# Optimization experiments

Measured on AMD Instinct MI355X. Metric: run time of the kernel, lower is better.

The kernel has to match this reference:

```python
import jax, jax.numpy as jnp
import numpy as np

N_NODES = 16384
D_IN = 256
D_OUT = 256
AVG_DEG = 32


def setup_inputs() -> dict:
    key = jax.random.key(0)
    kx, ka, kw, kb = jax.random.split(key, 4)
    x = jax.random.normal(kx, (N_NODES, D_IN), dtype=jnp.float32)
    # Binary dense adjacency with average degree ~AVG_DEG (matches `adj[i] > 0` usage).
    adj = (jax.random.uniform(ka, (N_NODES, N_NODES)) < (AVG_DEG / N_NODES)).astype(jnp.float32)
    # nn.Linear(2*in_features, out_features): weight [out, 2*in], bias [out]
    W = jax.random.normal(kw, (D_OUT, 2 * D_IN), dtype=jnp.float32) * (1.0 / np.sqrt(2 * D_IN))
    b = jnp.zeros((D_OUT,), dtype=jnp.float32)
    return {"x": x, "adj": adj, "W": W, "b": b, "sample_size": 10}


def reference(x, adj, W, b, sample_size):
    # Vectorized equivalent of the per-node loop:
    # sample min(deg, sample_size) neighbors uniformly without replacement,
    # mean-aggregate, concat with self features, linear + relu.
    key = jax.random.key(42)
    noise = jax.random.uniform(key, adj.shape)            # [N, N]
    # Gumbel-top-k trick: top-k uniform scores over neighbors == uniform sample w/o replacement.
    scores = jnp.where(adj > 0, noise, -jnp.inf)
    top_scores, top_idx = jax.lax.top_k(scores, sample_size)  # [N, k]
    valid = jnp.isfinite(top_scores)                          # [N, k] false where deg < k
    feats = x[top_idx] * valid[..., None].astype(x.dtype)     # [N, k, d]
    cnt = valid.sum(axis=-1, keepdims=True).astype(x.dtype)   # [N, 1]
    agg = feats.sum(axis=1) / jnp.maximum(cnt, 1.0)           # mean; zeros if no neighbors
    h = jnp.concatenate([x, agg], axis=-1)                    # [N, 2d]
    return jax.nn.relu(h @ W.T + b)
```

## Files before the change

kernel.cpp:

```cpp
#include <hip/hip_runtime.h>
#include <hip/hip_bf16.h>
#include <stdint.h>

#define N_NODES 16384
#define D_IN    256
#define D_OUT   256
#define K_SAMP  10
#define HALF_FLAT (1u << 27)

#define JAX_PARTITIONABLE 1

typedef __attribute__((ext_vector_type(4))) float  f32x4;
typedef __attribute__((ext_vector_type(8))) short  bf16x8;
typedef __attribute__((ext_vector_type(4))) int    i32x4;

__device__ __forceinline__ uint32_t rotl32(uint32_t x, int r) {
    return (x << r) | (x >> (32 - r));
}

__device__ __forceinline__ uint32_t jax_noise_bits(uint32_t r, uint32_t c) {
    const uint32_t i  = (r << 14) | c;
    const uint32_t k0 = 0u, k1 = 42u;
    const uint32_t k2 = 42u ^ 0x1BD11BDAu;
    uint32_t x0, x1;
#if JAX_PARTITIONABLE
    x0 = 0u;
    x1 = i;
#else
    const bool lo = (i < HALF_FLAT);
    x0 = lo ? i : (i - HALF_FLAT);
    x1 = lo ? (i + HALF_FLAT) : i;
#endif
    x0 += k0; x1 += k1;
#define TFR4(a,b,cc,d) \
    x0 += x1; x1 = rotl32(x1,a);  x1 ^= x0; \
    x0 += x1; x1 = rotl32(x1,b);  x1 ^= x0; \
    x0 += x1; x1 = rotl32(x1,cc); x1 ^= x0; \
    x0 += x1; x1 = rotl32(x1,d);  x1 ^= x0;
    TFR4(13,15,26,6);   x0 += k1; x1 += k2 + 1u;
    TFR4(17,29,16,24);  x0 += k2; x1 += k0 + 2u;
    TFR4(13,15,26,6);   x0 += k0; x1 += k1 + 3u;
    TFR4(17,29,16,24);  x0 += k1; x1 += k2 + 4u;
    TFR4(13,15,26,6);   x0 += k2; x1 += k0 + 5u;
#undef TFR4
#if JAX_PARTITIONABLE
    return x0 ^ x1;
#else
    return (i < HALF_FLAT) ? x0 : x1;
#endif
}

__device__ __forceinline__ unsigned short f2bfbits(float f) {
    __hip_bfloat16 h = __float2bfloat16(f);
    return *(unsigned short*)&h;
}

__global__ __launch_bounds__(256) void k_agg(
    const float* __restrict__ x, const float* __restrict__ adj,
    const float* __restrict__ W, unsigned short* __restrict__ Wb,
    unsigned short* __restrict__ h)
{
    const int t    = threadIdx.x;
    const int lane = t & 63;
    const int w    = t >> 6;
    const int r    = blockIdx.x * 4 + w;

    if (blockIdx.x < 128) {
        int i = (blockIdx.x * 256 + t) * 4;
        f32x4 v = *(const f32x4*)(W + i);
        ushort4 u;
        u.x = f2bfbits(v[0]); u.y = f2bfbits(v[1]);
        u.z = f2bfbits(v[2]); u.w = f2bfbits(v[3]);
        *(ushort4*)(Wb + i) = u;
    }

    __shared__ unsigned short candc[4][128];

    const i32x4* rowp = (const i32x4*)(adj + (size_t)r * N_NODES);
    int nc = 0;
    #pragma unroll 8
    for (int it = 0; it < 64; ++it) {
        i32x4 v = __builtin_nontemporal_load(rowp + it * 64 + lane);
        uint32_t any = (uint32_t)v[0] | (uint32_t)v[1] | (uint32_t)v[2] | (uint32_t)v[3];
        unsigned long long m4 = __ballot(any != 0u);
        if (m4) {
            int cb = (it * 64 + lane) * 4;
            #pragma unroll
            for (int j = 0; j < 4; ++j) {
                unsigned long long mask = __ballot(v[j] != 0);
                if (mask) {
                    if (v[j] != 0) {
                        int below = __builtin_amdgcn_mbcnt_hi(
                            (uint32_t)(mask >> 32),
                            __builtin_amdgcn_mbcnt_lo((uint32_t)mask, 0));
                        int slot = nc + below;
                        if (slot < 128) candc[w][slot] = (unsigned short)(cb + j);
                    }
                    nc += __popcll(mask);
                }
            }
        }
    }
    __syncthreads();
    if (nc > 128) nc = 128;

    unsigned long long k0 = 0ull, k1 = 0ull;
    if (lane < nc) {
        uint32_t c   = candc[w][lane];
        uint32_t u23 = jax_noise_bits((uint32_t)r, c) >> 9;
        k0 = ((((unsigned long long)u23) << 14) | (unsigned long long)(16383u - c)) + 1ull;
    }
    if (64 + lane < nc) {
        uint32_t c   = candc[w][64 + lane];
        uint32_t u23 = jax_noise_bits((uint32_t)r, c) >> 9;
        k1 = ((((unsigned long long)u23) << 14) | (unsigned long long)(16383u - c)) + 1ull;
    }

    const int m = nc < K_SAMP ? nc : K_SAMP;
    f32x4 acc = {0.f, 0.f, 0.f, 0.f};
    for (int s = 0; s < m; ++s) {
        unsigned long long my = k0 > k1 ? k0 : k1;
        #pragma unroll
        for (int o = 1; o < 64; o <<= 1) {
            unsigned long long other = __shfl_xor(my, o);
            if (other > my) my = other;
        }
        if (k0 == my) k0 = 0ull; else if (k1 == my) k1 = 0ull;
        const int col = 16383 - (int)((my - 1ull) & 0x3FFFull);
        f32x4 xv = *(const f32x4*)(x + (size_t)col * D_IN + lane * 4);
        acc += xv;
    }
    const float inv = (m > 0) ? 1.0f / (float)m : 0.0f;

    f32x4 sv = *(const f32x4*)(x + (size_t)r * D_IN + lane * 4);
    ushort4 us, ua;
    us.x = f2bfbits(sv[0]);        us.y = f2bfbits(sv[1]);
    us.z = f2bfbits(sv[2]);        us.w = f2bfbits(sv[3]);
    ua.x = f2bfbits(acc[0] * inv); ua.y = f2bfbits(acc[1] * inv);
    ua.z = f2bfbits(acc[2] * inv); ua.w = f2bfbits(acc[3] * inv);
    unsigned short* hr = h + (size_t)r * (2 * D_IN);
    *(ushort4*)(hr + lane * 4)         = us;
    *(ushort4*)(hr + D_IN + lane * 4)  = ua;
}

#define BM 64
#define BN 64
#define BK 64

__global__ __launch_bounds__(256) void k_gemm(
    const unsigned short* __restrict__ h, const unsigned short* __restrict__ Wb,
    const float* __restrict__ bias, float* __restrict__ out)
{
    __shared__ short As[2][BM * BK];
    __shared__ short Bs[2][BN * BK];

    const int t    = threadIdx.x;
    const int lane = t & 63;
    const int wv   = t >> 6;
    const int wr   = wv >> 1;
    const int wc   = wv & 1;
    const int m0   = blockIdx.x * BM;
    const int n0   = blockIdx.y * BN;
    const int lr   = lane & 15;
    const int lk   = lane >> 4;

    f32x4 acc[2][2] = {};

    const short* hA = (const short*)h;
    const short* wB = (const short*)Wb;

    const int q0  = t, q1 = t + 256;
    const int r0  = q0 >> 3, c0 = q0 & 7;
    const int r1  = q1 >> 3, c1 = q1 & 7;
    const int ba0 = (r0 * 128 + c0 * 16) ^ ((r0 & 7) << 4);
    const int ba1 = (r1 * 128 + c1 * 16) ^ ((r1 & 7) << 4);

    {
        i32x4 a0 = *(const i32x4*)(hA + (size_t)(m0 + r0) * 512 + c0 * 8);
        i32x4 a1 = *(const i32x4*)(hA + (size_t)(m0 + r1) * 512 + c1 * 8);
        i32x4 b0 = *(const i32x4*)(wB + (size_t)(n0 + r0) * 512 + c0 * 8);
        i32x4 b1 = *(const i32x4*)(wB + (size_t)(n0 + r1) * 512 + c1 * 8);
        *(i32x4*)((char*)&As[0][0] + ba0) = a0;
        *(i32x4*)((char*)&As[0][0] + ba1) = a1;
        *(i32x4*)((char*)&Bs[0][0] + ba0) = b0;
        *(i32x4*)((char*)&Bs[0][0] + ba1) = b1;
    }
    __syncthreads();

    for (int tt = 0; tt < 8; ++tt) {
        const int cur = tt & 1;
        i32x4 a0, a1, b0, b1;
        if (tt < 7) {
            const int k0n = (tt + 1) * BK;
            a0 = *(const i32x4*)(hA + (size_t)(m0 + r0) * 512 + k0n + c0 * 8);
            a1 = *(const i32x4*)(hA + (size_t)(m0 + r1) * 512 + k0n + c1 * 8);
            b0 = *(const i32x4*)(wB + (size_t)(n0 + r0) * 512 + k0n + c0 * 8);
            b1 = *(const i32x4*)(wB + (size_t)(n0 + r1) * 512 + k0n + c1 * 8);
        }

        #pragma unroll
        for (int kk = 0; kk < BK; kk += 32) {
            bf16x8 af[2], bf[2];
            #pragma unroll
            for (int mi = 0; mi < 2; ++mi) {
                int row = wr * 32 + mi * 16 + lr;
                int ba = (row * 128 + (kk + lk * 8) * 2) ^ ((row & 7) << 4);
                af[mi] = *(const bf16x8*)((const char*)&As[cur][0] + ba);
            }
            #pragma unroll
            for (int ni = 0; ni < 2; ++ni) {
                int row = wc * 32 + ni * 16 + lr;
                int ba = (row * 128 + (kk + lk * 8) * 2) ^ ((row & 7) << 4);
                bf[ni] = *(const bf16x8*)((const char*)&Bs[cur][0] + ba);
            }
            #pragma unroll
            for (int mi = 0; mi < 2; ++mi)
                #pragma unroll
                for (int ni = 0; ni < 2; ++ni)
                    acc[mi][ni] = __builtin_amdgcn_mfma_f32_16x16x32_bf16(
                        af[mi], bf[ni], acc[mi][ni], 0, 0, 0);
        }

        if (tt < 7) {
            const int nxt = cur ^ 1;
            *(i32x4*)((char*)&As[nxt][0] + ba0) = a0;
            *(i32x4*)((char*)&As[nxt][0] + ba1) = a1;
            *(i32x4*)((char*)&Bs[nxt][0] + ba0) = b0;
            *(i32x4*)((char*)&Bs[nxt][0] + ba1) = b1;
        }
        __syncthreads();
    }

    #pragma unroll
    for (int mi = 0; mi < 2; ++mi) {
        #pragma unroll
        for (int ni = 0; ni < 2; ++ni) {
            int col = n0 + wc * 32 + ni * 16 + lr;
            float bv = bias[col];
            #pragma unroll
            for (int j = 0; j < 4; ++j) {
                int rowg = m0 + wr * 32 + mi * 16 + lk * 4 + j;
                float v = acc[mi][ni][j] + bv;
                out[(size_t)rowg * D_OUT + col] = v > 0.0f ? v : 0.0f;
            }
        }
    }
}

extern "C" void kernel_launch(void* const* d_in, const int* in_sizes, int n_in,
                              void* d_out, int out_size, void* d_ws, size_t ws_size,
                              hipStream_t stream) {
    (void)in_sizes; (void)n_in; (void)out_size; (void)ws_size;
    const float* x   = (const float*)d_in[0];
    const float* adj = (const float*)d_in[1];
    const float* W   = (const float*)d_in[2];
    const float* b   = (const float*)d_in[3];

    unsigned short* hbuf = (unsigned short*)d_ws;
    unsigned short* Wb   = (unsigned short*)((char*)d_ws + (size_t)N_NODES * 512 * 2);
    float* out = (float*)d_out;

    hipLaunchKernelGGL(k_agg,  dim3(N_NODES / 4), dim3(256), 0, stream, x, adj, W, Wb, hbuf);
    hipLaunchKernelGGL(k_gemm, dim3(N_NODES / BM, D_OUT / BN), dim3(256), 0, stream,
                       hbuf, Wb, b, out);
}
```

Measured before the change: 214.1 us.

## Convert W to bf16 inside GEMM loads and add nontemporal hints

The separate fp32-to-bf16 conversion of W in the aggregation kernel is removed; the GEMM now loads fp32 W directly and converts it while staging into shared memory. The self-feature load moves earlier and an unneeded __syncthreads is dropped (each wave reads only its own candc slice). The h loads and output stores now use nontemporal hints. The GEMM reads twice as many bytes for W and does redundant conversions across blocks, but W is small and cached, and the aggregation kernel, which dominates on the 1 GiB adjacency scan, loses some work.

Result: no change. 217.9 us (+1.8%).

```diff
diff --git a/kernel.cpp b/kernel.cpp
--- a/kernel.cpp
+++ b/kernel.cpp
@@ -55,9 +55,17 @@
     return *(unsigned short*)&h;
 }
 
+__device__ __forceinline__ i32x4 cvt8bf(f32x4 a, f32x4 b) {
+    i32x4 r;
+    r[0] = (int)((uint32_t)f2bfbits(a[0]) | ((uint32_t)f2bfbits(a[1]) << 16));
+    r[1] = (int)((uint32_t)f2bfbits(a[2]) | ((uint32_t)f2bfbits(a[3]) << 16));
+    r[2] = (int)((uint32_t)f2bfbits(b[0]) | ((uint32_t)f2bfbits(b[1]) << 16));
+    r[3] = (int)((uint32_t)f2bfbits(b[2]) | ((uint32_t)f2bfbits(b[3]) << 16));
+    return r;
+}
+
 __global__ __launch_bounds__(256) void k_agg(
     const float* __restrict__ x, const float* __restrict__ adj,
-    const float* __restrict__ W, unsigned short* __restrict__ Wb,
     unsigned short* __restrict__ h)
 {
     const int t    = threadIdx.x;
@@ -65,15 +73,6 @@
     const int w    = t >> 6;
     const int r    = blockIdx.x * 4 + w;
 
-    if (blockIdx.x < 128) {
-        int i = (blockIdx.x * 256 + t) * 4;
-        f32x4 v = *(const f32x4*)(W + i);
-        ushort4 u;
-        u.x = f2bfbits(v[0]); u.y = f2bfbits(v[1]);
-        u.z = f2bfbits(v[2]); u.w = f2bfbits(v[3]);
-        *(ushort4*)(Wb + i) = u;
-    }
-
     __shared__ unsigned short candc[4][128];
 
     const i32x4* rowp = (const i32x4*)(adj + (size_t)r * N_NODES);
@@ -82,8 +81,7 @@
     for (int it = 0; it < 64; ++it) {
         i32x4 v = __builtin_nontemporal_load(rowp + it * 64 + lane);
         uint32_t any = (uint32_t)v[0] | (uint32_t)v[1] | (uint32_t)v[2] | (uint32_t)v[3];
-        unsigned long long m4 = __ballot(any != 0u);
-        if (m4) {
+        if (__ballot(any != 0u)) {
             int cb = (it * 64 + lane) * 4;
             #pragma unroll
             for (int j = 0; j < 4; ++j) {
@@ -101,8 +99,9 @@
             }
         }
     }
-    __syncthreads();
     if (nc > 128) nc = 128;
+
+    f32x4 sv = *(const f32x4*)(x + (size_t)r * D_IN + lane * 4);
 
     unsigned long long k0 = 0ull, k1 = 0ull;
     if (lane < nc) {
@@ -132,7 +131,6 @@
     }
     const float inv = (m > 0) ? 1.0f / (float)m : 0.0f;
 
-    f32x4 sv = *(const f32x4*)(x + (size_t)r * D_IN + lane * 4);
     ushort4 us, ua;
     us.x = f2bfbits(sv[0]);        us.y = f2bfbits(sv[1]);
     us.z = f2bfbits(sv[2]);        us.w = f2bfbits(sv[3]);
@@ -148,7 +146,7 @@
 #define BK 64
 
 __global__ __launch_bounds__(256) void k_gemm(
-    const unsigned short* __restrict__ h, const unsigned short* __restrict__ Wb,
+    const unsigned short* __restrict__ h, const float* __restrict__ W,
     const float* __restrict__ bias, float* __restrict__ out)
 {
     __shared__ short As[2][BM * BK];
@@ -167,7 +165,6 @@
     f32x4 acc[2][2] = {};
 
     const short* hA = (const short*)h;
-    const short* wB = (const short*)Wb;
 
     const int q0  = t, q1 = t + 256;
     const int r0  = q0 >> 3, c0 = q0 & 7;
@@ -176,26 +173,35 @@
     const int ba1 = (r1 * 128 + c1 * 16) ^ ((r1 & 7) << 4);
 
     {
-        i32x4 a0 = *(const i32x4*)(hA + (size_t)(m0 + r0) * 512 + c0 * 8);
-        i32x4 a1 = *(const i32x4*)(hA + (size_t)(m0 + r1) * 512 + c1 * 8);
-        i32x4 b0 = *(const i32x4*)(wB + (size_t)(n0 + r0) * 512 + c0 * 8);
-        i32x4 b1 = *(const i32x4*)(wB + (size_t)(n0 + r1) * 512 + c1 * 8);
+        i32x4 a0 = __builtin_nontemporal_load(
+            (const i32x4*)(hA + (size_t)(m0 + r0) * 512 + c0 * 8));
+        i32x4 a1 = __builtin_nontemporal_load(
+            (const i32x4*)(hA + (size_t)(m0 + r1) * 512 + c1 * 8));
+        f32x4 w0a = *(const f32x4*)(W + (size_t)(n0 + r0) * 512 + c0 * 8);
+        f32x4 w0b = *(const f32x4*)(W + (size_t)(n0 + r0) * 512 + c0 * 8 + 4);
+        f32x4 w1a = *(const f32x4*)(W + (size_t)(n0 + r1) * 512 + c1 * 8);
+        f32x4 w1b = *(const f32x4*)(W + (size_t)(n0 + r1) * 512 + c1 * 8 + 4);
         *(i32x4*)((char*)&As[0][0] + ba0) = a0;
         *(i32x4*)((char*)&As[0][0] + ba1) = a1;
-        *(i32x4*)((char*)&Bs[0][0] + ba0) = b0;
-        *(i32x4*)((char*)&Bs[0][0] + ba1) = b1;
+        *(i32x4*)((char*)&Bs[0][0] + ba0) = cvt8bf(w0a, w0b);
+        *(i32x4*)((char*)&Bs[0][0] + ba1) = cvt8bf(w1a, w1b);
     }
     __syncthreads();
 
     for (int tt = 0; tt < 8; ++tt) {
         const int cur = tt & 1;
-        i32x4 a0, a1, b0, b1;
+        i32x4 a0, a1;
+        f32x4 w0a, w0b, w1a, w1b;
         if (tt < 7) {
             const int k0n = (tt + 1) * BK;
-            a0 = *(const i32x4*)(hA + (size_t)(m0 + r0) * 512 + k0n + c0 * 8);
-            a1 = *(const i32x4*)(hA + (size_t)(m0 + r1) * 512 + k0n + c1 * 8);
-            b0 = *(const i32x4*)(wB + (size_t)(n0 + r0) * 512 + k0n + c0 * 8);
-            b1 = *(const i32x4*)(wB + (size_t)(n0 + r1) * 512 + k0n + c1 * 8);
+            a0 = __builtin_nontemporal_load(
+                (const i32x4*)(hA + (size_t)(m0 + r0) * 512 + k0n + c0 * 8));
+            a1 = __builtin_nontemporal_load(
+                (const i32x4*)(hA + (size_t)(m0 + r1) * 512 + k0n + c1 * 8));
+            w0a = *(const f32x4*)(W + (size_t)(n0 + r0) * 512 + k0n + c0 * 8);
+            w0b = *(const f32x4*)(W + (size_t)(n0 + r0) * 512 + k0n + c0 * 8 + 4);
+            w1a = *(const f32x4*)(W + (size_t)(n0 + r1) * 512 + k0n + c1 * 8);
+            w1b = *(const f32x4*)(W + (size_t)(n0 + r1) * 512 + k0n + c1 * 8 + 4);
         }
 
         #pragma unroll
@@ -225,8 +231,8 @@
             const int nxt = cur ^ 1;
             *(i32x4*)((char*)&As[nxt][0] + ba0) = a0;
             *(i32x4*)((char*)&As[nxt][0] + ba1) = a1;
-            *(i32x4*)((char*)&Bs[nxt][0] + ba0) = b0;
-            *(i32x4*)((char*)&Bs[nxt][0] + ba1) = b1;
+            *(i32x4*)((char*)&Bs[nxt][0] + ba0) = cvt8bf(w0a, w0b);
+            *(i32x4*)((char*)&Bs[nxt][0] + ba1) = cvt8bf(w1a, w1b);
         }
         __syncthreads();
     }
@@ -241,7 +247,8 @@
             for (int j = 0; j < 4; ++j) {
                 int rowg = m0 + wr * 32 + mi * 16 + lk * 4 + j;
                 float v = acc[mi][ni][j] + bv;
-                out[(size_t)rowg * D_OUT + col] = v > 0.0f ? v : 0.0f;
+                v = v > 0.0f ? v : 0.0f;
+                __builtin_nontemporal_store(v, out + (size_t)rowg * D_OUT + col);
             }
         }
     }
@@ -257,10 +264,9 @@
     const float* b   = (const float*)d_in[3];
 
     unsigned short* hbuf = (unsigned short*)d_ws;
-    unsigned short* Wb   = (unsigned short*)((char*)d_ws + (size_t)N_NODES * 512 * 2);
     float* out = (float*)d_out;
 
-    hipLaunchKernelGGL(k_agg,  dim3(N_NODES / 4), dim3(256), 0, stream, x, adj, W, Wb, hbuf);
+    hipLaunchKernelGGL(k_agg,  dim3(N_NODES / 4), dim3(256), 0, stream, x, adj, hbuf);
     hipLaunchKernelGGL(k_gemm, dim3(N_NODES / BM, D_OUT / BN), dim3(256), 0, stream,
-                       hbuf, Wb, b, out);
-}
+                       hbuf, W, b, out);
+}
```
